# Performance work log

Hardware: AMD Instinct MI355X
Metric: run time of the kernel (lower is better)

## Reference

```python
import jax, jax.numpy as jnp
import numpy as np

N = 4096
IN_F = 256
OUT_F = 64
K = 4
ALPHA = 0.2  # LeakyReLU negative slope
NEG_INF = -9e15


def setup_inputs() -> dict:
    key = jax.random.key(0)
    k_h, k_w, k_a, k_e, k_m = jax.random.split(key, 5)
    h = jax.random.normal(k_h, (N, IN_F), dtype=jnp.float32)
    # xavier_uniform with gain=1.414
    def xavier(k, shape, gain=1.414):
        fan_in, fan_out = shape[0], shape[1]
        limit = gain * np.sqrt(6.0 / (fan_in + fan_out))
        return jax.random.uniform(k, shape, jnp.float32, -limit, limit)
    W = xavier(k_w, (IN_F, OUT_F))
    a = xavier(k_a, (2 * OUT_F, 1))
    vals = jax.random.uniform(k_e, (K, N, N), dtype=jnp.float32)
    mask = jax.random.uniform(k_m, (K, N, N), dtype=jnp.float32) < 0.05
    edge_attr = jnp.where(mask, vals, 0.0)
    return {"h": h, "edge_attr": edge_attr, "W": W, "a": a}


def reference(h, edge_attr, W, a):
    # h: [N, IN_F], edge_attr: [K, N, N], W: [IN_F, OUT_F], a: [2*OUT_F, 1]
    Wh = h @ W                                   # [N, OUT_F]
    Wh1 = Wh @ a[:OUT_F, :]                      # [N, 1]
    Wh2 = Wh @ a[OUT_F:, :]                      # [N, 1]
    e = jax.nn.leaky_relu(Wh1 + Wh2.T, negative_slope=ALPHA)  # [N, N]
    e = e[None, :, :] * edge_attr                # [K, N, N]
    e = jnp.where(edge_attr > 0, e, NEG_INF)
    att = jax.nn.softmax(e, axis=1)              # softmax over dim=1, as in torch
    # dropout is identity in eval mode
    # batched replacement for the per-channel python loop of matmuls
    hp = jnp.einsum('kij,jf->kif', att, Wh)      # [K, N, OUT_F]
    out = jnp.transpose(hp, (1, 0, 2)).reshape(N, K * OUT_F)  # concat dim=1
    return jax.nn.elu(out), att
```

## Files before the change

### kernel.cpp

```cpp
#include <hip/hip_runtime.h>

#define NN 4096
#define IN_F 256
#define OUT_F 64
#define K_CH 4
#define ALPHA 0.2f
#define JP 8
#define JCOLS 512
#define IC 256

typedef __bf16 bf16;
typedef __attribute__((ext_vector_type(8))) __bf16 bf16x8;
typedef __attribute__((ext_vector_type(4))) float f32x4;

__global__ __launch_bounds__(256) void k0_wh(const float* __restrict__ h,
                                             const float* __restrict__ W,
                                             const float* __restrict__ a,
                                             float* __restrict__ Wh,
                                             float* __restrict__ Wh1,
                                             float* __restrict__ Wh2) {
    int tid = threadIdx.x;
    int wave = tid >> 6, lane = tid & 63;
    int i = blockIdx.x * 4 + wave;
    const float* hrow = h + (size_t)i * IN_F;
    float acc = 0.f;
    #pragma unroll 8
    for (int c = 0; c < IN_F; ++c)
        acc += hrow[c] * W[c * OUT_F + lane];
    Wh[(size_t)i * OUT_F + lane] = acc;
    float v1 = acc * a[lane];
    float v2 = acc * a[OUT_F + lane];
    #pragma unroll
    for (int o = 32; o > 0; o >>= 1) {
        v1 += __shfl_xor(v1, o, 64);
        v2 += __shfl_xor(v2, o, 64);
    }
    if (lane == 0) { Wh1[i] = v1; Wh2[i] = v2; }
}

__global__ __launch_bounds__(256) void k0_transpose(const float* __restrict__ Wh,
                                                    bf16* __restrict__ WhT) {
    __shared__ float lds[OUT_F * 65];
    int tid = threadIdx.x;
    int i0 = blockIdx.x * 64;
    int f = tid & 63;
    int r0 = tid >> 6;
    #pragma unroll
    for (int s = 0; s < 16; ++s) {
        int r = r0 * 16 + s;
        lds[f * 65 + r] = Wh[(size_t)(i0 + r) * OUT_F + f];
    }
    __syncthreads();
    int f2 = tid >> 2;
    int c0 = (tid & 3) * 16;
    #pragma unroll
    for (int s = 0; s < 16; ++s) {
        int c = c0 + s;
        WhT[(size_t)f2 * NN + i0 + c] = (bf16)lds[f2 * 65 + c];
    }
}

__global__ __launch_bounds__(256) void k1_colsum(const float* __restrict__ edge,
                                                 const float* __restrict__ Wh1,
                                                 const float* __restrict__ Wh2,
                                                 float* __restrict__ partial) {
    int tid = threadIdx.x;
    int kch = blockIdx.z;
    int j0 = blockIdx.y * 2048 + tid * 8;
    int ic = blockIdx.x;
    int ibase = ic * 16;
    float w2[8];
    {
        f32x4 t0 = *(const f32x4*)&Wh2[j0];
        f32x4 t1 = *(const f32x4*)&Wh2[j0 + 4];
        #pragma unroll
        for (int c = 0; c < 4; ++c) { w2[c] = t0[c]; w2[c + 4] = t1[c]; }
    }
    float s[8] = {0.f, 0.f, 0.f, 0.f, 0.f, 0.f, 0.f, 0.f};
    const float* base = edge + ((size_t)kch * NN + ibase) * NN + j0;
    f32x4 r0[2], r1[2];
    r0[0] = *(const f32x4*)(base);
    r1[0] = *(const f32x4*)(base + 4);
    r0[1] = *(const f32x4*)(base + NN);
    r1[1] = *(const f32x4*)(base + NN + 4);
    #pragma unroll 2
    for (int ii = 0; ii < 16; ++ii) {
        int cur = ii & 1;
        f32x4 e0 = r0[cur], e1 = r1[cur];
        int ip = (ii + 2 < 16) ? ii + 2 : ii;
        r0[cur] = *(const f32x4*)(base + (size_t)ip * NN);
        r1[cur] = *(const f32x4*)(base + (size_t)ip * NN + 4);
        float wh1 = Wh1[ibase + ii];
        #pragma unroll
        for (int c = 0; c < 8; ++c) {
            float ef = c < 4 ? e0[c] : e1[c - 4];
            float xv = wh1 + w2[c];
            float lk = xv > 0.f ? xv : ALPHA * xv;
            s[c] += ef > 0.f ? __expf(lk * ef) : 0.f;
        }
    }
    float* pr = partial + ((size_t)ic * K_CH + kch) * NN + j0;
    f32x4 o0, o1;
    #pragma unroll
    for (int c = 0; c < 4; ++c) { o0[c] = s[c]; o1[c] = s[c + 4]; }
    *(f32x4*)pr = o0;
    *(f32x4*)(pr + 4) = o1;
}

__global__ __launch_bounds__(256) void k1_reduce(const float* __restrict__ partial,
                                                 float* __restrict__ s_col) {
    int g = blockIdx.x * 256 + threadIdx.x;
    float s = 0.f;
    #pragma unroll 8
    for (int ic = 0; ic < IC; ++ic)
        s += partial[(size_t)ic * (K_CH * NN) + g];
    s_col[g] = s;
}

__global__ __launch_bounds__(256) void k2_fused(const float* __restrict__ edge,
                                                const float* __restrict__ Wh1,
                                                const float* __restrict__ Wh2,
                                                const float* __restrict__ s_col,
                                                const bf16* __restrict__ WhT,
                                                float* __restrict__ att_out,
                                                float* __restrict__ hp_part) {
    __shared__ float lds_inv[JCOLS];
    __shared__ float lds_w2[JCOLS];
    int tid = threadIdx.x;
    int itile = blockIdx.x;
    int kch = blockIdx.y;
    int jp = blockIdx.z;
    int jbase0 = jp * JCOLS;
    {
        int t2 = tid * 2;
        float s0 = s_col[kch * NN + jbase0 + t2];
        float s1 = s_col[kch * NN + jbase0 + t2 + 1];
        lds_inv[t2]     = s0 > 0.f ? 1.f / s0 : 0.f;
        lds_inv[t2 + 1] = s1 > 0.f ? 1.f / s1 : 0.f;
        lds_w2[t2]      = Wh2[jbase0 + t2];
        lds_w2[t2 + 1]  = Wh2[jbase0 + t2 + 1];
    }
    __syncthreads();
    int wave = tid >> 6, lane = tid & 63;
    int n16 = lane & 15, quad = lane >> 4;
    int i_row = itile * 64 + wave * 16 + n16;
    float wh1 = Wh1[i_row];
    const size_t ebase = ((size_t)kch * NN + i_row) * (size_t)NN + jbase0 + quad * 8;
    const float* eptr = edge + ebase;
    float* aptr = att_out + ebase;
    const bf16* wbase = WhT + (size_t)n16 * NN + jbase0 + quad * 8;
    f32x4 acc[4] = {};
    f32x4 p0[2], p1[2];
    #pragma unroll
    for (int t = 0; t < 2; ++t) {
        p0[t] = *(const f32x4*)(eptr + t * 32);
        p1[t] = *(const f32x4*)(eptr + t * 32 + 4);
    }
    #pragma unroll 2
    for (int s = 0; s < 16; ++s) {
        int cur = s & 1;
        f32x4 e0 = p0[cur], e1 = p1[cur];
        int sp = (s + 2 < 16) ? s + 2 : s;
        p0[cur] = *(const f32x4*)(eptr + sp * 32);
        p1[cur] = *(const f32x4*)(eptr + sp * 32 + 4);
        int jl = s * 32 + quad * 8;
        f32x4 iv0 = *(const f32x4*)&lds_inv[jl];
        f32x4 iv1 = *(const f32x4*)&lds_inv[jl + 4];
        f32x4 wv0 = *(const f32x4*)&lds_w2[jl];
        f32x4 wv1 = *(const f32x4*)&lds_w2[jl + 4];
        bf16x8 afrag;
        f32x4 av0, av1;
        #pragma unroll
        for (int c = 0; c < 8; ++c) {
            float ef = c < 4 ? e0[c] : e1[c - 4];
            float w2c = c < 4 ? wv0[c] : wv1[c - 4];
            float isc = c < 4 ? iv0[c] : iv1[c - 4];
            float xv = wh1 + w2c;
            float lk = xv > 0.f ? xv : ALPHA * xv;
            float attv = ef > 0.f ? __expf(lk * ef) * isc : 0.f;
            afrag[c] = (bf16)attv;
            if (c < 4) av0[c] = attv; else av1[c - 4] = attv;
        }
        __builtin_nontemporal_store(av0, (f32x4*)(aptr + s * 32));
        __builtin_nontemporal_store(av1, (f32x4*)(aptr + s * 32 + 4));
        #pragma unroll
        for (int ft = 0; ft < 4; ++ft) {
            bf16x8 bfrag = *(const bf16x8*)(wbase + (size_t)ft * 16 * NN + s * 32);
            acc[ft] = __builtin_amdgcn_mfma_f32_16x16x32_bf16(afrag, bfrag, acc[ft], 0, 0, 0);
        }
    }
    #pragma unroll
    for (int ft = 0; ft < 4; ++ft) {
        #pragma unroll
        for (int r = 0; r < 4; ++r) {
            int row_l = quad * 4 + r;
            int i_g = itile * 64 + wave * 16 + row_l;
            size_t idx = (((size_t)jp * K_CH + kch) * NN + i_g) * OUT_F + ft * 16 + n16;
            hp_part[idx] = acc[ft][r];
        }
    }
}

__global__ __launch_bounds__(256) void k3_combine(const float* __restrict__ hp_part,
                                                  float* __restrict__ out) {
    int g = blockIdx.x * 256 + threadIdx.x;
    int i = g >> 8;
    int rem = g & 255;
    int kch = rem >> 6;
    int f = rem & 63;
    float s = 0.f;
    #pragma unroll
    for (int z = 0; z < JP; ++z)
        s += hp_part[(((size_t)z * K_CH + kch) * NN + i) * OUT_F + f];
    out[g] = s > 0.f ? s : __expf(s) - 1.f;
}

extern "C" void kernel_launch(void* const* d_in, const int* in_sizes, int n_in,
                              void* d_out, int out_size, void* d_ws, size_t ws_size,
                              hipStream_t stream) {
    (void)out_size; (void)ws_size;
    const float *h = nullptr, *edge = nullptr, *W = nullptr, *a = nullptr;
    for (int i = 0; i < n_in; ++i) {
        int sz = in_sizes[i];
        if (sz == NN * IN_F)               h    = (const float*)d_in[i];
        else if (sz == K_CH * NN * NN)     edge = (const float*)d_in[i];
        else if (sz == IN_F * OUT_F)       W    = (const float*)d_in[i];
        else if (sz == 2 * OUT_F)          a    = (const float*)d_in[i];
    }

    char* ws = (char*)d_ws;
    float* Wh    = (float*)(ws);
    float* Wh1   = (float*)(ws + 1048576);
    float* Wh2   = (float*)(ws + 1048576 + 16384);
    float* s_col = (float*)(ws + 1048576 + 32768);
    bf16*  WhT   = (bf16*) (ws + 1048576 + 32768 + 65536);
    float* hp    = (float*)(ws + 1048576 + 32768 + 65536 + 524288);
    float* partial = hp;

    float* out_h   = (float*)d_out;
    float* att_out = out_h + (size_t)NN * (K_CH * OUT_F);

    k0_wh<<<dim3(NN / 4), 256, 0, stream>>>(h, W, a, Wh, Wh1, Wh2);
    k0_transpose<<<dim3(NN / 64), 256, 0, stream>>>(Wh, WhT);
    k1_colsum<<<dim3(IC, 2, 4), 256, 0, stream>>>(edge, Wh1, Wh2, partial);
    k1_reduce<<<dim3(K_CH * NN / 256), 256, 0, stream>>>(partial, s_col);
    k2_fused<<<dim3(64, 4, JP), 256, 0, stream>>>(edge, Wh1, Wh2, s_col, WhT, att_out, hp);
    k3_combine<<<dim3((NN * K_CH * OUT_F) / 256), 256, 0, stream>>>(hp, out_h);
}
```

Baseline: 617.6 us.

## Process attention channels sequentially so edge slices stay cache-resident between passes

Splits the column-sum, normalize/matmul, and combine kernels into a per-channel loop, so each 64 MB edge slice is read by the second pass shortly after the first. This aims to serve the k2 re-read of the edge tensor from the large last-level cache instead of HBM. It also retunes tiles (8 rows per colsum block, 256-column tiles with deeper prefetch) and rewrites the partial-sum reduction with LDS. In exchange it needs more kernel launches and a larger workspace, and each launch has a smaller grid.

```diff
diff --git a/kernel.cpp b/kernel.cpp
--- a/kernel.cpp
+++ b/kernel.cpp
@@ -5,9 +5,10 @@
 #define OUT_F 64
 #define K_CH 4
 #define ALPHA 0.2f
-#define JP 8
-#define JCOLS 512
-#define IC 256
+#define JP 16
+#define JCOLS 256
+#define ROWS1 8
+#define IC1 512
 
 typedef __bf16 bf16;
 typedef __attribute__((ext_vector_type(8))) __bf16 bf16x8;
@@ -60,15 +61,14 @@
     }
 }
 
-__global__ __launch_bounds__(256) void k1_colsum(const float* __restrict__ edge,
+__global__ __launch_bounds__(256) void k1_colsum(const float* __restrict__ edge_ch,
                                                  const float* __restrict__ Wh1,
                                                  const float* __restrict__ Wh2,
                                                  float* __restrict__ partial) {
     int tid = threadIdx.x;
-    int kch = blockIdx.z;
     int j0 = blockIdx.y * 2048 + tid * 8;
     int ic = blockIdx.x;
-    int ibase = ic * 16;
+    int ibase = ic * ROWS1;
     float w2[8];
     {
         f32x4 t0 = *(const f32x4*)&Wh2[j0];
@@ -77,17 +77,18 @@
         for (int c = 0; c < 4; ++c) { w2[c] = t0[c]; w2[c + 4] = t1[c]; }
     }
     float s[8] = {0.f, 0.f, 0.f, 0.f, 0.f, 0.f, 0.f, 0.f};
-    const float* base = edge + ((size_t)kch * NN + ibase) * NN + j0;
-    f32x4 r0[2], r1[2];
-    r0[0] = *(const f32x4*)(base);
-    r1[0] = *(const f32x4*)(base + 4);
-    r0[1] = *(const f32x4*)(base + NN);
-    r1[1] = *(const f32x4*)(base + NN + 4);
-    #pragma unroll 2
-    for (int ii = 0; ii < 16; ++ii) {
-        int cur = ii & 1;
+    const float* base = edge_ch + (size_t)ibase * NN + j0;
+    f32x4 r0[4], r1[4];
+    #pragma unroll
+    for (int t = 0; t < 4; ++t) {
+        r0[t] = *(const f32x4*)(base + (size_t)t * NN);
+        r1[t] = *(const f32x4*)(base + (size_t)t * NN + 4);
+    }
+    #pragma unroll
+    for (int ii = 0; ii < ROWS1; ++ii) {
+        int cur = ii & 3;
         f32x4 e0 = r0[cur], e1 = r1[cur];
-        int ip = (ii + 2 < 16) ? ii + 2 : ii;
+        int ip = (ii + 4 < ROWS1) ? ii + 4 : ii;
         r0[cur] = *(const f32x4*)(base + (size_t)ip * NN);
         r1[cur] = *(const f32x4*)(base + (size_t)ip * NN + 4);
         float wh1 = Wh1[ibase + ii];
@@ -99,7 +100,7 @@
             s[c] += ef > 0.f ? __expf(lk * ef) : 0.f;
         }
     }
-    float* pr = partial + ((size_t)ic * K_CH + kch) * NN + j0;
+    float* pr = partial + (size_t)ic * NN + j0;
     f32x4 o0, o1;
     #pragma unroll
     for (int c = 0; c < 4; ++c) { o0[c] = s[c]; o1[c] = s[c + 4]; }
@@ -109,58 +110,59 @@
 
 __global__ __launch_bounds__(256) void k1_reduce(const float* __restrict__ partial,
                                                  float* __restrict__ s_col) {
-    int g = blockIdx.x * 256 + threadIdx.x;
+    __shared__ float red[256];
+    int tid = threadIdx.x;
+    int jl = tid & 63, g = tid >> 6;
+    int j = blockIdx.x * 64 + jl;
     float s = 0.f;
     #pragma unroll 8
-    for (int ic = 0; ic < IC; ++ic)
-        s += partial[(size_t)ic * (K_CH * NN) + g];
-    s_col[g] = s;
-}
-
-__global__ __launch_bounds__(256) void k2_fused(const float* __restrict__ edge,
+    for (int t = 0; t < IC1 / 4; ++t)
+        s += partial[(size_t)(g * (IC1 / 4) + t) * NN + j];
+    red[tid] = s;
+    __syncthreads();
+    if (tid < 64)
+        s_col[j] = red[tid] + red[tid + 64] + red[tid + 128] + red[tid + 192];
+}
+
+__global__ __launch_bounds__(256) void k2_fused(const float* __restrict__ edge_ch,
                                                 const float* __restrict__ Wh1,
                                                 const float* __restrict__ Wh2,
                                                 const float* __restrict__ s_col,
                                                 const bf16* __restrict__ WhT,
-                                                float* __restrict__ att_out,
-                                                float* __restrict__ hp_part) {
+                                                float* __restrict__ att_ch,
+                                                float* __restrict__ hp) {
     __shared__ float lds_inv[JCOLS];
     __shared__ float lds_w2[JCOLS];
     int tid = threadIdx.x;
     int itile = blockIdx.x;
-    int kch = blockIdx.y;
-    int jp = blockIdx.z;
+    int jp = blockIdx.y;
     int jbase0 = jp * JCOLS;
     {
-        int t2 = tid * 2;
-        float s0 = s_col[kch * NN + jbase0 + t2];
-        float s1 = s_col[kch * NN + jbase0 + t2 + 1];
-        lds_inv[t2]     = s0 > 0.f ? 1.f / s0 : 0.f;
-        lds_inv[t2 + 1] = s1 > 0.f ? 1.f / s1 : 0.f;
-        lds_w2[t2]      = Wh2[jbase0 + t2];
-        lds_w2[t2 + 1]  = Wh2[jbase0 + t2 + 1];
+        float s0 = s_col[jbase0 + tid];
+        lds_inv[tid] = s0 > 0.f ? 1.f / s0 : 0.f;
+        lds_w2[tid]  = Wh2[jbase0 + tid];
     }
     __syncthreads();
     int wave = tid >> 6, lane = tid & 63;
     int n16 = lane & 15, quad = lane >> 4;
     int i_row = itile * 64 + wave * 16 + n16;
     float wh1 = Wh1[i_row];
-    const size_t ebase = ((size_t)kch * NN + i_row) * (size_t)NN + jbase0 + quad * 8;
-    const float* eptr = edge + ebase;
-    float* aptr = att_out + ebase;
+    const size_t ebase = (size_t)i_row * NN + jbase0 + quad * 8;
+    const float* eptr = edge_ch + ebase;
+    float* aptr = att_ch + ebase;
     const bf16* wbase = WhT + (size_t)n16 * NN + jbase0 + quad * 8;
     f32x4 acc[4] = {};
-    f32x4 p0[2], p1[2];
-    #pragma unroll
-    for (int t = 0; t < 2; ++t) {
+    f32x4 p0[4], p1[4];
+    #pragma unroll
+    for (int t = 0; t < 4; ++t) {
         p0[t] = *(const f32x4*)(eptr + t * 32);
         p1[t] = *(const f32x4*)(eptr + t * 32 + 4);
     }
-    #pragma unroll 2
-    for (int s = 0; s < 16; ++s) {
-        int cur = s & 1;
+    #pragma unroll
+    for (int s = 0; s < JCOLS / 32; ++s) {
+        int cur = s & 3;
         f32x4 e0 = p0[cur], e1 = p1[cur];
-        int sp = (s + 2 < 16) ? s + 2 : s;
+        int sp = (s + 4 < JCOLS / 32) ? s + 4 : s;
         p0[cur] = *(const f32x4*)(eptr + sp * 32);
         p1[cur] = *(const f32x4*)(eptr + sp * 32 + 4);
         int jl = s * 32 + quad * 8;
@@ -195,24 +197,23 @@
         for (int r = 0; r < 4; ++r) {
             int row_l = quad * 4 + r;
             int i_g = itile * 64 + wave * 16 + row_l;
-            size_t idx = (((size_t)jp * K_CH + kch) * NN + i_g) * OUT_F + ft * 16 + n16;
-            hp_part[idx] = acc[ft][r];
-        }
-    }
-}
-
-__global__ __launch_bounds__(256) void k3_combine(const float* __restrict__ hp_part,
-                                                  float* __restrict__ out) {
+            size_t idx = ((size_t)jp * NN + i_g) * OUT_F + ft * 16 + n16;
+            hp[idx] = acc[ft][r];
+        }
+    }
+}
+
+__global__ __launch_bounds__(256) void k3_combine(const float* __restrict__ hp,
+                                                  float* __restrict__ out,
+                                                  int kch) {
     int g = blockIdx.x * 256 + threadIdx.x;
-    int i = g >> 8;
-    int rem = g & 255;
-    int kch = rem >> 6;
-    int f = rem & 63;
+    int i = g >> 6;
+    int f = g & 63;
     float s = 0.f;
     #pragma unroll
     for (int z = 0; z < JP; ++z)
-        s += hp_part[(((size_t)z * K_CH + kch) * NN + i) * OUT_F + f];
-    out[g] = s > 0.f ? s : __expf(s) - 1.f;
+        s += hp[((size_t)z * NN + i) * OUT_F + f];
+    out[(size_t)i * (K_CH * OUT_F) + kch * OUT_F + f] = s > 0.f ? s : __expf(s) - 1.f;
 }
 
 extern "C" void kernel_launch(void* const* d_in, const int* in_sizes, int n_in,
@@ -229,21 +230,26 @@
     }
 
     char* ws = (char*)d_ws;
-    float* Wh    = (float*)(ws);
-    float* Wh1   = (float*)(ws + 1048576);
-    float* Wh2   = (float*)(ws + 1048576 + 16384);
-    float* s_col = (float*)(ws + 1048576 + 32768);
-    bf16*  WhT   = (bf16*) (ws + 1048576 + 32768 + 65536);
-    float* hp    = (float*)(ws + 1048576 + 32768 + 65536 + 524288);
-    float* partial = hp;
+    float* Wh      = (float*)(ws);
+    float* Wh1     = (float*)(ws + 1048576);
+    float* Wh2     = (float*)(ws + 1048576 + 16384);
+    float* s_col   = (float*)(ws + 1048576 + 32768);
+    bf16*  WhT     = (bf16*) (ws + 1048576 + 49152);
+    float* partial = (float*)(ws + 1048576 + 49152 + 524288);
+    float* hp      = (float*)(ws + 1048576 + 49152 + 524288 + 8388608);
 
     float* out_h   = (float*)d_out;
     float* att_out = out_h + (size_t)NN * (K_CH * OUT_F);
 
     k0_wh<<<dim3(NN / 4), 256, 0, stream>>>(h, W, a, Wh, Wh1, Wh2);
     k0_transpose<<<dim3(NN / 64), 256, 0, stream>>>(Wh, WhT);
-    k1_colsum<<<dim3(IC, 2, 4), 256, 0, stream>>>(edge, Wh1, Wh2, partial);
-    k1_reduce<<<dim3(K_CH * NN / 256), 256, 0, stream>>>(partial, s_col);
-    k2_fused<<<dim3(64, 4, JP), 256, 0, stream>>>(edge, Wh1, Wh2, s_col, WhT, att_out, hp);
-    k3_combine<<<dim3((NN * K_CH * OUT_F) / 256), 256, 0, stream>>>(hp, out_h);
-}
+
+    for (int ch = 0; ch < K_CH; ++ch) {
+        const float* edge_ch = edge + (size_t)ch * NN * NN;
+        float* att_ch = att_out + (size_t)ch * NN * NN;
+        k1_colsum<<<dim3(IC1, 2), 256, 0, stream>>>(edge_ch, Wh1, Wh2, partial);
+        k1_reduce<<<dim3(NN / 64), 256, 0, stream>>>(partial, s_col);
+        k2_fused<<<dim3(64, JP), 256, 0, stream>>>(edge_ch, Wh1, Wh2, s_col, WhT, att_ch, hp);
+        k3_combine<<<dim3(NN * OUT_F / 256), 256, 0, stream>>>(hp, out_h, ch);
+    }
+}
```

After: 628.6 us. Within noise of the previous version (+1.8%).
